# Performance work log

Hardware: AMD Instinct MI355X
Metric: run time of the kernel (lower is better)

## Reference

```python
import jax, jax.numpy as jnp
import numpy as np

B, C, H, W = 4, 128, 512, 512
K = 512          # num_kpt
NMS_R = 3        # nms_radius -> 7x7 window
NMS_ITER = 2


def _maxpool(x, r):
    # torch nn.MaxPool2d(kernel=2r+1, stride=1, padding=r) pads with -inf semantics
    return jax.lax.reduce_window(
        x, -jnp.inf, jax.lax.max,
        window_dimensions=(1, 1, 2 * r + 1, 2 * r + 1),
        window_strides=(1, 1, 1, 1),
        padding=((0, 0), (0, 0), (r, r), (r, r)))


def simple_nms(scores, r=NMS_R, iters=NMS_ITER):
    zeros = jnp.zeros_like(scores)
    max_mask = scores == _maxpool(scores, r)
    for _ in range(iters):
        supp_mask = _maxpool(max_mask.astype(scores.dtype), r) > 0
        supp_scores = jnp.where(supp_mask, zeros, scores)
        new_max_mask = supp_scores == _maxpool(supp_scores, r)
        max_mask = max_mask | (new_max_mask & ~supp_mask)
    return jnp.where(max_mask, scores, zeros)


def setup_inputs() -> dict:
    key = jax.random.key(0)
    k1, k2, k3 = jax.random.split(key, 3)
    score_bev = jax.random.uniform(k1, (B, 1, H, W), dtype=jnp.float32)
    feature_bev = jax.random.normal(k2, (B, C, H, W), dtype=jnp.float32)
    points = jax.random.normal(k3, (B, 4, H, W), dtype=jnp.float32)
    return {"score_bev": score_bev, "feature_bev": feature_bev, "points": points}


def reference(score_bev, feature_bev, points):
    # points[:,2]=0, points[:,3]=1 as in torch forward
    pts = points.at[:, 2].set(0.0).at[:, 3].set(1.0)

    nms = simple_nms(score_bev)                      # [B,1,H,W]
    s = score_bev[:, 0]                              # [B,H,W]
    sm = nms[:, 0]
    mask = (s == sm) & (s > 0)                       # NMS-surviving positive maxima

    # per-image top-k over valid candidates (invalid -> -1 sentinel, scores > 0)
    flat = jnp.where(mask, s, -1.0).reshape(B, H * W)
    _, idx = jax.lax.top_k(flat, K)                  # [B,K], sorted descending
    u, v = idx // W, idx % W                         # pixel coords

    kpts = jnp.take_along_axis(pts.reshape(B, 4, H * W), idx[:, None, :], axis=2)
    kpts = kpts.transpose(0, 2, 1)                   # [B,K,4]
    feas_kpt = jnp.take_along_axis(feature_bev.reshape(B, C, H * W), idx[:, None, :], axis=2)  # [B,C,K]
    pixels_kpt = jnp.stack([u, v], axis=-1)          # [B,K,2] int
    return kpts, feas_kpt, pixels_kpt
```

## Files before the change

### kernel.cpp

```cpp
#include <hip/hip_runtime.h>
#include <stdint.h>
#include <math.h>

#define BB 4
#define HH 512
#define WW 512
#define HWW (HH*WW)
#define CC 128
#define KK 512
#define SELCAP 2048
#define NBIN 8192
#define NPADK 512

#define TILE 64
#define HALO 15
#define TS 94
#define SWL 104
#define NT 1024
#define TCAP 512
#define NW2 16

typedef unsigned int uint;
typedef unsigned long long u64;

__device__ __forceinline__ float4 ldsf4(const float* p, int o){ return *(const float4*)(p + o); }

#define COLMAX7V(src, o, cm)                                                  \
    { float4 c0=ldsf4(src,(o)-3*SWL), c1=ldsf4(src,(o)-2*SWL), c2=ldsf4(src,(o)-SWL), \
             c3=ldsf4(src,(o)),       c4=ldsf4(src,(o)+SWL),   c5=ldsf4(src,(o)+2*SWL), \
             c6=ldsf4(src,(o)+3*SWL);                                         \
      cm.x=fmaxf(fmaxf(fmaxf(c0.x,c1.x),fmaxf(c2.x,c3.x)),fmaxf(fmaxf(c4.x,c5.x),c6.x)); \
      cm.y=fmaxf(fmaxf(fmaxf(c0.y,c1.y),fmaxf(c2.y,c3.y)),fmaxf(fmaxf(c4.y,c5.y),c6.y)); \
      cm.z=fmaxf(fmaxf(fmaxf(c0.z,c1.z),fmaxf(c2.z,c3.z)),fmaxf(fmaxf(c4.z,c5.z),c6.z)); \
      cm.w=fmaxf(fmaxf(fmaxf(c0.w,c1.w),fmaxf(c2.w,c3.w)),fmaxf(fmaxf(c4.w,c5.w),c6.w)); }

#define ROWMAXV(dst, src, Y0, NROW, G0, NG)                                   \
    for (int i = tid; i < (NROW)*(NG); i += NT){                              \
        int y = (Y0) + i/(NG);                                                \
        int o = y*SWL + (G0) + 4*(i%(NG)) + 4;                                \
        float4 va = ldsf4(src, o-4), vb = ldsf4(src, o), vc = ldsf4(src, o+4);\
        float m2a=fmaxf(va.y,va.z), m2b=fmaxf(va.w,vb.x), m2c=fmaxf(vb.y,vb.z),\
              m2d=fmaxf(vb.w,vc.x), m2e=fmaxf(vc.y,vc.z);                     \
        float4 r;                                                             \
        r.x = fmaxf(fmaxf(m2a,m2b), fmaxf(m2c, vb.w));                        \
        r.y = fmaxf(fmaxf(va.z,m2b), fmaxf(m2c, m2d));                        \
        r.z = fmaxf(fmaxf(m2b,m2c), fmaxf(m2d, vc.y));                        \
        r.w = fmaxf(fmaxf(vb.x,m2c), fmaxf(m2d, m2e));                        \
        *(float4*)((dst) + o) = r;                                            \
    }                                                                         \
    __syncthreads();

#define ROWORV(dst, src, Y0, NROW, G0, NG)                                    \
    for (int i = tid; i < (NROW)*(NG); i += NT){                              \
        int y = (Y0) + i/(NG);                                                \
        int o = y*SWL + (G0) + 4*(i%(NG)) + 4;                                \
        uint u0 = *(const uint*)((src)+o-4), u1 = *(const uint*)((src)+o),    \
             u2 = *(const uint*)((src)+o+4);                                  \
        u64 lo = (u64)u0 | ((u64)u1 << 32);                                   \
        uint r = (uint)(lo>>8) | (uint)(lo>>16) | (uint)(lo>>24) | (uint)(lo>>32) \
               | ((uint)(lo>>40)|(u2<<24)) | ((uint)(lo>>48)|(u2<<16))        \
               | ((uint)(lo>>56)|(u2<<8));                                    \
        *(uint*)((dst)+o) = r;                                                \
    }                                                                         \
    __syncthreads();

#define COLSUPPV(Y0, NROW, G0, NG)                                            \
    for (int i = tid; i < (NROW)*(NG); i += NT){                              \
        int y = (Y0) + i/(NG);                                                \
        int o = y*SWL + (G0) + 4*(i%(NG)) + 4;                                \
        uint v = *(const uint*)(T+o-3*SWL) | *(const uint*)(T+o-2*SWL)        \
               | *(const uint*)(T+o-SWL)   | *(const uint*)(T+o)              \
               | *(const uint*)(T+o+SWL)   | *(const uint*)(T+o+2*SWL)        \
               | *(const uint*)(T+o+3*SWL);                                   \
        *(uint*)(P + o) = v;                                                  \
        float4 s4 = ldsf4(S, o);                                              \
        float4 a;                                                             \
        a.x = (v & 0xffu)       ? 0.0f : s4.x;                                \
        a.y = (v & 0xff00u)     ? 0.0f : s4.y;                                \
        a.z = (v & 0xff0000u)   ? 0.0f : s4.z;                                \
        a.w = (v & 0xff000000u) ? 0.0f : s4.w;                                \
        *(float4*)(A + o) = a;                                                \
    }                                                                         \
    __syncthreads();

__global__ __launch_bounds__(NT) void nms_fused_k(const float* __restrict__ sc,
        float* __restrict__ cs, int* __restrict__ ci, int* __restrict__ cnt){
    __shared__ __align__(16) float S[TS*SWL];
    __shared__ __align__(16) float A[TS*SWL];
    __shared__ __align__(16) float Bf[TS*SWL];
    __shared__ __align__(16) unsigned char M[TS*SWL];
    __shared__ __align__(16) unsigned char T[TS*SWL];
    __shared__ __align__(16) unsigned char P[TS*SWL];
    __shared__ float lsc[TCAP];
    __shared__ int   lidx[TCAP];
    __shared__ int   lcnt;

    const int tid = threadIdx.x;
    const int bb = blockIdx.x >> 6;
    const int t  = blockIdx.x & 63;
    const int ty = t >> 3, tx = t & 7;
    const int oy = ty * TILE - HALO, ox = tx * TILE - HALO;
    const float* sb = sc + (size_t)bb * HWW;
    const float QNAN = __int_as_float(0x7fc00000);

    if (tid == 0) lcnt = 0;

    for (int i = tid; i < TS*SWL; i += NT){
        int y = i / SWL, x = i - y*SWL;
        int gy = oy + y, gx = ox + x - 4;
        float v = QNAN;
        if ((unsigned)gy < (unsigned)HH && (unsigned)gx < (unsigned)WW)
            v = sb[(gy << 9) + gx];
        S[i] = v;
    }
    __syncthreads();

    ROWMAXV(A, S, 0, 94, 0, 23)
    for (int i = tid; i < 88*23; i += NT){
        int y = 3 + i/23;
        int o = y*SWL + 4*(i%23) + 4;
        float4 cm; COLMAX7V(A, o, cm);
        float4 s4 = ldsf4(S, o);
        uint m = (s4.x==cm.x ?1u:0u) | (s4.y==cm.y ?0x100u:0u)
               | (s4.z==cm.z ?0x10000u:0u) | (s4.w==cm.w ?0x1000000u:0u);
        *(uint*)(M + o) = m;
    }
    __syncthreads();

    ROWORV(T, M, 3, 88, 4, 21)
    COLSUPPV(6, 82, 4, 21)
    ROWMAXV(Bf, A, 6, 82, 8, 20)
    for (int i = tid; i < 76*20; i += NT){
        int y = 9 + i/20;
        int o = y*SWL + 8 + 4*(i%20) + 4;
        float4 cm; COLMAX7V(Bf, o, cm);
        float4 a4 = ldsf4(A, o);
        uint p4 = *(const uint*)(P+o);
        uint nm = (a4.x==cm.x ?1u:0u)|(a4.y==cm.y ?0x100u:0u)
                | (a4.z==cm.z ?0x10000u:0u)|(a4.w==cm.w ?0x1000000u:0u);
        uint m4 = *(const uint*)(M+o);
        *(uint*)(M+o) = m4 | (nm & ~p4);
    }
    __syncthreads();

    ROWORV(T, M, 9, 76, 12, 18)
    COLSUPPV(12, 70, 12, 18)
    ROWMAXV(Bf, A, 12, 70, 12, 17)

    for (int i = tid; i < 64*17; i += NT){
        int y = 15 + i/17;
        int xg = 12 + 4*(i%17);
        int o = y*SWL + xg + 4;
        float4 cm; COLMAX7V(Bf, o, cm);
        float4 a4 = ldsf4(A, o), s4 = ldsf4(S, o);
        uint p4 = *(const uint*)(P+o), m4 = *(const uint*)(M+o);
        float sa[4] = {s4.x, s4.y, s4.z, s4.w};
        float aa[4] = {a4.x, a4.y, a4.z, a4.w};
        float ca[4] = {cm.x, cm.y, cm.z, cm.w};
        #pragma unroll
        for (int j = 0; j < 4; ++j){
            int x = xg + j;
            bool fm = ((m4 >> (8*j)) & 1u) || ((aa[j]==ca[j]) && !((p4 >> (8*j)) & 1u));
            if ((unsigned)(x - 15) < 64u && fm && sa[j] > 0.0f){
                int p = atomicAdd(&lcnt, 1);
                if (p < TCAP){ lsc[p] = sa[j]; lidx[p] = ((oy+y) << 9) + (ox+x); }
            }
        }
    }
    __syncthreads();

    int nl = lcnt; if (nl > TCAP) nl = TCAP;
    const int seg = bb * 64 + t;
    if (tid == 0) cnt[seg] = nl;
    float* os = cs + (size_t)seg * TCAP;
    int*   oi = ci + (size_t)seg * TCAP;
    for (int i = tid; i < nl; i += NT){ os[i] = lsc[i]; oi[i] = lidx[i]; }
}


__device__ __forceinline__ uint fxbin(float v){
    return ((uint)(v * 8388608.0f)) >> 10;
}

__global__ __launch_bounds__(NT) void selgather_k(
        const float* __restrict__ cs, const int* __restrict__ ci, const int* __restrict__ cnt,
        const float* __restrict__ pts, const float* __restrict__ feat,
        float* __restrict__ out){
    __shared__ int  hist[NBIN];
    __shared__ __align__(16) u64 keys[SELCAP + 4];
    __shared__ int  segc[64];
    __shared__ int  wsum[16];
    __shared__ int  sidx[KK];
    __shared__ uint sh_Tbits;
    __shared__ int  sh_bin, sh_kneed, sh_n, selCnt, bcnt;

    const int blk = blockIdx.x;
    const int b = blk >> 6, slice = blk & 63;
    const int tid = threadIdx.x;
    const int wv = tid >> 6, lane = tid & 63;

    {
        int4* h4 = (int4*)hist;
        for (int i = tid; i < NBIN/4; i += NT) h4[i] = make_int4(0,0,0,0);
    }
    if (tid < 64){ int c = cnt[b*64 + tid]; segc[tid] = (c > TCAP) ? TCAP : c; }
    if (tid == 0){ selCnt = 0; bcnt = 0; sh_Tbits = 1u; }
    __syncthreads();

    #pragma unroll
    for (int ss = 0; ss < 4; ++ss){
        int s = wv*4 + ss;
        int c = segc[s];
        const float* ps = cs + (size_t)(b*64 + s) * TCAP;
        for (int i = lane; i < c; i += 64)
            atomicAdd(&hist[fxbin(ps[i])], 1);
    }
    __syncthreads();

    int hh[8];
    {
        int4 h0 = *(int4*)&hist[tid*8], h1 = *(int4*)&hist[tid*8 + 4];
        hh[0]=h0.x; hh[1]=h0.y; hh[2]=h0.z; hh[3]=h0.w;
        hh[4]=h1.x; hh[5]=h1.y; hh[6]=h1.z; hh[7]=h1.w;
    }
    int s8 = hh[0]+hh[1]+hh[2]+hh[3]+hh[4]+hh[5]+hh[6]+hh[7];
    int suf = s8;
    #pragma unroll
    for (int off = 1; off < 64; off <<= 1){
        int v = __shfl_down(suf, off);
        if (lane + off < 64) suf += v;
    }
    if (lane == 0) wsum[wv] = suf;
    __syncthreads();
    int W = 0, tot = 0;
    #pragma unroll
    for (int w2 = 0; w2 < 16; ++w2){ int v = wsum[w2]; tot += v; if (w2 > wv) W += v; }
    if (tid == 0) sh_n = tot;
    int G = W + (suf - s8);
    if (tot >= KK && G < KK && G + s8 >= KK){
        int cum = G;
        #pragma unroll
        for (int k = 7; k >= 0; --k){
            if (cum + hh[k] >= KK){ sh_bin = tid*8 + k; sh_kneed = KK - cum; break; }
            cum += hh[k];
        }
    }
    __syncthreads();
    const int n = sh_n;

    uint Tbits = 1u;
    if (n >= KK){
        const int bstar = sh_bin, kneed = sh_kneed;
        #pragma unroll
        for (int ss = 0; ss < 4; ++ss){
            int s = wv*4 + ss;
            int c = segc[s];
            const float* ps = cs + (size_t)(b*64 + s) * TCAP;
            for (int i = lane; i < c; i += 64){
                float v = ps[i];
                if ((int)fxbin(v) == bstar){
                    int p = atomicAdd(&bcnt, 1);
                    if (p < SELCAP) keys[p] = (u64)__float_as_uint(v);
                }
            }
        }
        __syncthreads();
        int m = bcnt; if (m > SELCAP) m = SELCAP;
        if (tid < m){
            u64 mine = keys[tid];
            int gt = 0, ge = 0;
            for (int j = 0; j < m; ++j){
                u64 v = keys[j];
                gt += (v > mine) ? 1 : 0;
                ge += (v >= mine) ? 1 : 0;
            }
            if (gt < kneed && kneed <= ge) sh_Tbits = (uint)mine;
        }
        __syncthreads();
        Tbits = sh_Tbits;
    }

    #pragma unroll
    for (int ss = 0; ss < 4; ++ss){
        int s = wv*4 + ss;
        int c = segc[s];
        const float* ps = cs + (size_t)(b*64 + s) * TCAP;
        const int*   pi = ci + (size_t)(b*64 + s) * TCAP;
        for (int i0 = 0; i0 < c; i0 += 64){
            int i = i0 + lane;
            bool hit = false; uint bits = 0;
            if (i < c){ bits = __float_as_uint(ps[i]); hit = (bits >= Tbits); }
            u64 m = __ballot(hit);
            if (!m) continue;
            int wbase = 0;
            if (lane == 0) wbase = atomicAdd(&selCnt, (int)__popcll(m));
            wbase = __shfl(wbase, 0);
            if (hit){
                int p = wbase + (int)__popcll(m & ((1ull << lane) - 1ull));
                if (p < SELCAP) keys[p] = ((u64)bits << 32) | (uint)(~pi[i]);
            }
        }
    }
    __syncthreads();
    int ns = selCnt; if (ns > SELCAP) ns = SELCAP;
    for (int i = ns + tid; i < NPADK; i += NT) keys[i] = 0ull;
    __syncthreads();

    if (ns <= NPADK){
        u64 ck[8];
        #pragma unroll
        for (int r = 0; r < 8; ++r) ck[r] = keys[r*64 + lane];
        for (int t0 = 0; t0 < 32; ++t0){
            int t = wv*32 + t0;
            u64 my = keys[t];
            int c = 0;
            #pragma unroll
            for (int r = 0; r < 8; ++r) c += (ck[r] > my) ? 1 : 0;
            #pragma unroll
            for (int off = 1; off < 64; off <<= 1) c += __shfl_xor(c, off);
            if (lane == 0 && my != 0ull && c < KK)
                sidx[c] = (int)(~(uint)(my & 0xFFFFFFFFull));
        }
    } else {
        for (int i = tid; i < ns; i += NT){
            u64 my = keys[i];
            int rank = 0;
            for (int j = 0; j < ns; ++j) rank += (keys[j] > my) ? 1 : 0;
            if (rank < KK) sidx[rank] = (int)(~(uint)(my & 0xFFFFFFFFull));
        }
    }
    __syncthreads();

    if (ns < KK && tid == 0){
        int fill = ns;
        for (int idx = 0; idx < HWW && fill < KK; ++idx){
            bool inCand = false;
            for (int s = 0; s < 64 && !inCand; ++s){
                const int* pi = ci + (size_t)(b*64 + s) * TCAP;
                int c = segc[s];
                for (int i = 0; i < c; ++i) if (pi[i] == idx){ inCand = true; break; }
            }
            if (!inCand) sidx[fill++] = idx;
        }
    }
    __syncthreads();

    if (slice == 0){
        const float* pb = pts + (size_t)b * 4 * HWW;
        float* out0 = out + (size_t)b * KK * 4;
        float* out2 = out + (size_t)(BB * KK * 4 + BB * CC * KK) + (size_t)b * KK * 2;
        for (int k = tid; k < KK; k += NT){
            int idx = sidx[k];
            out0[k * 4 + 0] = pb[idx];
            out0[k * 4 + 1] = pb[HWW + idx];
            out0[k * 4 + 2] = 0.0f;
            out0[k * 4 + 3] = 1.0f;
            out2[k * 2 + 0] = (float)(idx >> 9);
            out2[k * 2 + 1] = (float)(idx & (WW - 1));
        }
    }
    {
        int j = slice * NT + tid;
        int c = j >> 9;
        int k = j & (KK - 1);
        float* out1 = out + (size_t)(BB * KK * 4) + (size_t)b * CC * KK;
        out1[j] = feat[(size_t)b * CC * HWW + (size_t)c * HWW + sidx[k]];
    }
}

extern "C" void kernel_launch(void* const* d_in, const int* in_sizes, int n_in,
                              void* d_out, int out_size, void* d_ws, size_t ws_size,
                              hipStream_t stream) {
    const float* s    = (const float*)d_in[0];
    const float* feat = (const float*)d_in[1];
    const float* pts  = (const float*)d_in[2];
    float* out = (float*)d_out;

    char* w = (char*)d_ws;
    float* cs  = (float*)w;  w += (size_t)BB * 64 * TCAP * 4;
    int*   ci  = (int*)w;    w += (size_t)BB * 64 * TCAP * 4;
    int*   cnt = (int*)w;    w += (size_t)BB * 64 * 4;

    nms_fused_k<<<BB * 64, NT, 0, stream>>>(s, cs, ci, cnt);
    selgather_k<<<BB * 64, NT, 0, stream>>>(cs, ci, cnt, pts, feat, out);
}
```

Measured before the change: 54.82 us.

## Use register sliding windows for row and column max/or passes in NMS

```diff
diff --git a/kernel.cpp b/kernel.cpp
--- a/kernel.cpp
+++ b/kernel.cpp
@@ -24,64 +24,62 @@
 typedef unsigned long long u64;
 
 __device__ __forceinline__ float4 ldsf4(const float* p, int o){ return *(const float4*)(p + o); }
-
-#define COLMAX7V(src, o, cm)                                                  \
-    { float4 c0=ldsf4(src,(o)-3*SWL), c1=ldsf4(src,(o)-2*SWL), c2=ldsf4(src,(o)-SWL), \
-             c3=ldsf4(src,(o)),       c4=ldsf4(src,(o)+SWL),   c5=ldsf4(src,(o)+2*SWL), \
-             c6=ldsf4(src,(o)+3*SWL);                                         \
-      cm.x=fmaxf(fmaxf(fmaxf(c0.x,c1.x),fmaxf(c2.x,c3.x)),fmaxf(fmaxf(c4.x,c5.x),c6.x)); \
-      cm.y=fmaxf(fmaxf(fmaxf(c0.y,c1.y),fmaxf(c2.y,c3.y)),fmaxf(fmaxf(c4.y,c5.y),c6.y)); \
-      cm.z=fmaxf(fmaxf(fmaxf(c0.z,c1.z),fmaxf(c2.z,c3.z)),fmaxf(fmaxf(c4.z,c5.z),c6.z)); \
-      cm.w=fmaxf(fmaxf(fmaxf(c0.w,c1.w),fmaxf(c2.w,c3.w)),fmaxf(fmaxf(c4.w,c5.w),c6.w)); }
-
-#define ROWMAXV(dst, src, Y0, NROW, G0, NG)                                   \
-    for (int i = tid; i < (NROW)*(NG); i += NT){                              \
-        int y = (Y0) + i/(NG);                                                \
-        int o = y*SWL + (G0) + 4*(i%(NG)) + 4;                                \
-        float4 va = ldsf4(src, o-4), vb = ldsf4(src, o), vc = ldsf4(src, o+4);\
-        float m2a=fmaxf(va.y,va.z), m2b=fmaxf(va.w,vb.x), m2c=fmaxf(vb.y,vb.z),\
-              m2d=fmaxf(vb.w,vc.x), m2e=fmaxf(vc.y,vc.z);                     \
-        float4 r;                                                             \
-        r.x = fmaxf(fmaxf(m2a,m2b), fmaxf(m2c, vb.w));                        \
-        r.y = fmaxf(fmaxf(va.z,m2b), fmaxf(m2c, m2d));                        \
-        r.z = fmaxf(fmaxf(m2b,m2c), fmaxf(m2d, vc.y));                        \
-        r.w = fmaxf(fmaxf(vb.x,m2c), fmaxf(m2d, m2e));                        \
-        *(float4*)((dst) + o) = r;                                            \
+__device__ __forceinline__ float4 f4max(float4 a, float4 b){
+    return make_float4(fmaxf(a.x,b.x), fmaxf(a.y,b.y), fmaxf(a.z,b.z), fmaxf(a.w,b.w));
+}
+
+#define ROWMAX_RUN(dst, src, Y0, NROW, G0, NG)                                \
+    { const int RUNS = ((NG) + 7) / 8;                                        \
+      for (int th = tid; th < (NROW)*RUNS; th += NT){                         \
+        int row = th / RUNS, u = th % RUNS;                                   \
+        int y = (Y0) + row, g0 = u*8;                                         \
+        int o0 = y*SWL + (G0) + 4*g0 + 4;                                     \
+        float4 Ax = ldsf4(src, o0-4), Bx = ldsf4(src, o0);                    \
+        _Pragma("unroll")                                                     \
+        for (int q = 0; q < 8; ++q){                                          \
+            if (g0 + q < (NG)){                                               \
+                int o = o0 + 4*q;                                             \
+                float4 Cx = ldsf4(src, o+4);                                  \
+                float m2a=fmaxf(Ax.y,Ax.z), m2b=fmaxf(Ax.w,Bx.x),             \
+                      m2c=fmaxf(Bx.y,Bx.z), m2d=fmaxf(Bx.w,Cx.x),             \
+                      m2e=fmaxf(Cx.y,Cx.z);                                   \
+                float4 r;                                                     \
+                r.x = fmaxf(fmaxf(m2a,m2b), fmaxf(m2c, Bx.w));                \
+                r.y = fmaxf(fmaxf(Ax.z,m2b), fmaxf(m2c, m2d));                \
+                r.z = fmaxf(fmaxf(m2b,m2c), fmaxf(m2d, Cx.y));                \
+                r.w = fmaxf(fmaxf(Bx.x,m2c), fmaxf(m2d, m2e));                \
+                *(float4*)((dst) + o) = r;                                    \
+                Ax = Bx; Bx = Cx;                                             \
+            }                                                                 \
+        }                                                                     \
+      }                                                                       \
     }                                                                         \
     __syncthreads();
 
-#define ROWORV(dst, src, Y0, NROW, G0, NG)                                    \
-    for (int i = tid; i < (NROW)*(NG); i += NT){                              \
-        int y = (Y0) + i/(NG);                                                \
-        int o = y*SWL + (G0) + 4*(i%(NG)) + 4;                                \
-        uint u0 = *(const uint*)((src)+o-4), u1 = *(const uint*)((src)+o),    \
-             u2 = *(const uint*)((src)+o+4);                                  \
-        u64 lo = (u64)u0 | ((u64)u1 << 32);                                   \
-        uint r = (uint)(lo>>8) | (uint)(lo>>16) | (uint)(lo>>24) | (uint)(lo>>32) \
-               | ((uint)(lo>>40)|(u2<<24)) | ((uint)(lo>>48)|(u2<<16))        \
-               | ((uint)(lo>>56)|(u2<<8));                                    \
-        *(uint*)((dst)+o) = r;                                                \
+#define ROWOR_RUN(dst, src, Y0, NROW, G0, NG)                                 \
+    { const int RUNS = ((NG) + 7) / 8;                                        \
+      for (int th = tid; th < (NROW)*RUNS; th += NT){                         \
+        int row = th / RUNS, u = th % RUNS;                                   \
+        int y = (Y0) + row, g0 = u*8;                                         \
+        int o0 = y*SWL + (G0) + 4*g0 + 4;                                     \
+        uint Au = *(const uint*)((src)+o0-4), Bu = *(const uint*)((src)+o0);  \
+        _Pragma("unroll")                                                     \
+        for (int q = 0; q < 8; ++q){                                          \
+            if (g0 + q < (NG)){                                               \
+                int o = o0 + 4*q;                                             \
+                uint Cu = *(const uint*)((src)+o+4);                          \
+                u64 lo = (u64)Au | ((u64)Bu << 32);                           \
+                uint r = (uint)(lo>>8) | (uint)(lo>>16) | (uint)(lo>>24)      \
+                       | (uint)(lo>>32) | ((uint)(lo>>40)|(Cu<<24))           \
+                       | ((uint)(lo>>48)|(Cu<<16)) | ((uint)(lo>>56)|(Cu<<8));\
+                *(uint*)((dst)+o) = r;                                        \
+                Au = Bu; Bu = Cu;                                             \
+            }                                                                 \
+        }                                                                     \
+      }                                                                       \
     }                                                                         \
     __syncthreads();
 
-#define COLSUPPV(Y0, NROW, G0, NG)                                            \
-    for (int i = tid; i < (NROW)*(NG); i += NT){                              \
-        int y = (Y0) + i/(NG);                                                \
-        int o = y*SWL + (G0) + 4*(i%(NG)) + 4;                                \
-        uint v = *(const uint*)(T+o-3*SWL) | *(const uint*)(T+o-2*SWL)        \
-               | *(const uint*)(T+o-SWL)   | *(const uint*)(T+o)              \
-               | *(const uint*)(T+o+SWL)   | *(const uint*)(T+o+2*SWL)        \
-               | *(const uint*)(T+o+3*SWL);                                   \
-        *(uint*)(P + o) = v;                                                  \
-        float4 s4 = ldsf4(S, o);                                              \
-        float4 a;                                                             \
-        a.x = (v & 0xffu)       ? 0.0f : s4.x;                                \
-        a.y = (v & 0xff00u)     ? 0.0f : s4.y;                                \
-        a.z = (v & 0xff0000u)   ? 0.0f : s4.z;                                \
-        a.w = (v & 0xff000000u) ? 0.0f : s4.w;                                \
-        *(float4*)(A + o) = a;                                                \
-    }                                                                         \
-    __syncthreads();
 
 __global__ __launch_bounds__(NT) void nms_fused_k(const float* __restrict__ sc,
         float* __restrict__ cs, int* __restrict__ ci, int* __restrict__ cnt){
@@ -115,56 +113,141 @@
     }
     __syncthreads();
 
-    ROWMAXV(A, S, 0, 94, 0, 23)
-    for (int i = tid; i < 88*23; i += NT){
-        int y = 3 + i/23;
-        int o = y*SWL + 4*(i%23) + 4;
-        float4 cm; COLMAX7V(A, o, cm);
-        float4 s4 = ldsf4(S, o);
-        uint m = (s4.x==cm.x ?1u:0u) | (s4.y==cm.y ?0x100u:0u)
-               | (s4.z==cm.z ?0x10000u:0u) | (s4.w==cm.w ?0x1000000u:0u);
-        *(uint*)(M + o) = m;
-    }
-    __syncthreads();
-
-    ROWORV(T, M, 3, 88, 4, 21)
-    COLSUPPV(6, 82, 4, 21)
-    ROWMAXV(Bf, A, 6, 82, 8, 20)
-    for (int i = tid; i < 76*20; i += NT){
-        int y = 9 + i/20;
-        int o = y*SWL + 8 + 4*(i%20) + 4;
-        float4 cm; COLMAX7V(Bf, o, cm);
-        float4 a4 = ldsf4(A, o);
-        uint p4 = *(const uint*)(P+o);
-        uint nm = (a4.x==cm.x ?1u:0u)|(a4.y==cm.y ?0x100u:0u)
-                | (a4.z==cm.z ?0x10000u:0u)|(a4.w==cm.w ?0x1000000u:0u);
-        uint m4 = *(const uint*)(M+o);
-        *(uint*)(M+o) = m4 | (nm & ~p4);
-    }
-    __syncthreads();
-
-    ROWORV(T, M, 9, 76, 12, 18)
-    COLSUPPV(12, 70, 12, 18)
-    ROWMAXV(Bf, A, 12, 70, 12, 17)
-
-    for (int i = tid; i < 64*17; i += NT){
-        int y = 15 + i/17;
-        int xg = 12 + 4*(i%17);
-        int o = y*SWL + xg + 4;
-        float4 cm; COLMAX7V(Bf, o, cm);
-        float4 a4 = ldsf4(A, o), s4 = ldsf4(S, o);
-        uint p4 = *(const uint*)(P+o), m4 = *(const uint*)(M+o);
-        float sa[4] = {s4.x, s4.y, s4.z, s4.w};
-        float aa[4] = {a4.x, a4.y, a4.z, a4.w};
-        float ca[4] = {cm.x, cm.y, cm.z, cm.w};
-        #pragma unroll
-        for (int j = 0; j < 4; ++j){
-            int x = xg + j;
-            bool fm = ((m4 >> (8*j)) & 1u) || ((aa[j]==ca[j]) && !((p4 >> (8*j)) & 1u));
-            if ((unsigned)(x - 15) < 64u && fm && sa[j] > 0.0f){
-                int p = atomicAdd(&lcnt, 1);
-                if (p < TCAP){ lsc[p] = sa[j]; lidx[p] = ((oy+y) << 9) + (ox+x); }
-            }
+    ROWMAX_RUN(A, S, 0, 94, 0, 23)
+
+    for (int th = tid; th < 11*23; th += NT){
+        int st = th / 23, g = th % 23;
+        int ys = 3 + st*8;
+        int xo = 4*g + 4;
+        float4 w0 = ldsf4(A,(ys-3)*SWL+xo), w1 = ldsf4(A,(ys-2)*SWL+xo),
+               w2 = ldsf4(A,(ys-1)*SWL+xo), w3 = ldsf4(A,(ys  )*SWL+xo),
+               w4 = ldsf4(A,(ys+1)*SWL+xo), w5 = ldsf4(A,(ys+2)*SWL+xo);
+        #pragma unroll
+        for (int r2 = 0; r2 < 8; ++r2){
+            int y = ys + r2;
+            float4 w6 = ldsf4(A,(y+3)*SWL+xo);
+            float4 cm = f4max(f4max(f4max(w0,w1),f4max(w2,w3)), f4max(f4max(w4,w5),w6));
+            float4 s4 = ldsf4(S, y*SWL+xo);
+            uint m = (s4.x==cm.x?1u:0u)|(s4.y==cm.y?0x100u:0u)
+                   | (s4.z==cm.z?0x10000u:0u)|(s4.w==cm.w?0x1000000u:0u);
+            *(uint*)(M + y*SWL+xo) = m;
+            w0=w1; w1=w2; w2=w3; w3=w4; w4=w5; w5=w6;
+        }
+    }
+    __syncthreads();
+
+    ROWOR_RUN(T, M, 3, 88, 4, 21)
+
+    for (int th = tid; th < 14*21; th += NT){
+        int st = th / 21, g = th % 21;
+        int ys = 6 + st*6;
+        int xo = 4*g + 8;
+        uint t0 = *(uint*)(T+(ys-3)*SWL+xo), t1 = *(uint*)(T+(ys-2)*SWL+xo),
+             t2 = *(uint*)(T+(ys-1)*SWL+xo), t3 = *(uint*)(T+(ys  )*SWL+xo),
+             t4 = *(uint*)(T+(ys+1)*SWL+xo), t5 = *(uint*)(T+(ys+2)*SWL+xo);
+        #pragma unroll
+        for (int r2 = 0; r2 < 6; ++r2){
+            int y = ys + r2;
+            if (y < 88){
+                uint t6 = *(uint*)(T+(y+3)*SWL+xo);
+                uint v = t0|t1|t2|t3|t4|t5|t6;
+                *(uint*)(P + y*SWL+xo) = v;
+                float4 s4 = ldsf4(S, y*SWL+xo);
+                float4 a;
+                a.x = (v & 0xffu)       ? 0.0f : s4.x;
+                a.y = (v & 0xff00u)     ? 0.0f : s4.y;
+                a.z = (v & 0xff0000u)   ? 0.0f : s4.z;
+                a.w = (v & 0xff000000u) ? 0.0f : s4.w;
+                *(float4*)(A + y*SWL+xo) = a;
+                t0=t1; t1=t2; t2=t3; t3=t4; t4=t5; t5=t6;
+            }
+        }
+    }
+    __syncthreads();
+
+    ROWMAX_RUN(Bf, A, 6, 82, 8, 20)
+
+    for (int th = tid; th < 19*20; th += NT){
+        int st = th / 20, g = th % 20;
+        int ys = 9 + st*4;
+        int xo = 4*g + 12;
+        float4 w0 = ldsf4(Bf,(ys-3)*SWL+xo), w1 = ldsf4(Bf,(ys-2)*SWL+xo),
+               w2 = ldsf4(Bf,(ys-1)*SWL+xo), w3 = ldsf4(Bf,(ys  )*SWL+xo),
+               w4 = ldsf4(Bf,(ys+1)*SWL+xo), w5 = ldsf4(Bf,(ys+2)*SWL+xo);
+        #pragma unroll
+        for (int r2 = 0; r2 < 4; ++r2){
+            int y = ys + r2;
+            float4 w6 = ldsf4(Bf,(y+3)*SWL+xo);
+            float4 cm = f4max(f4max(f4max(w0,w1),f4max(w2,w3)), f4max(f4max(w4,w5),w6));
+            float4 a4 = ldsf4(A, y*SWL+xo);
+            uint p4 = *(uint*)(P + y*SWL+xo);
+            uint nm = (a4.x==cm.x?1u:0u)|(a4.y==cm.y?0x100u:0u)
+                    | (a4.z==cm.z?0x10000u:0u)|(a4.w==cm.w?0x1000000u:0u);
+            uint m4 = *(uint*)(M + y*SWL+xo);
+            *(uint*)(M + y*SWL+xo) = m4 | (nm & ~p4);
+            w0=w1; w1=w2; w2=w3; w3=w4; w4=w5; w5=w6;
+        }
+    }
+    __syncthreads();
+
+    ROWOR_RUN(T, M, 9, 76, 12, 18)
+
+    for (int th = tid; th < 10*18; th += NT){
+        int st = th / 18, g = th % 18;
+        int ys = 12 + st*7;
+        int xo = 4*g + 16;
+        uint t0 = *(uint*)(T+(ys-3)*SWL+xo), t1 = *(uint*)(T+(ys-2)*SWL+xo),
+             t2 = *(uint*)(T+(ys-1)*SWL+xo), t3 = *(uint*)(T+(ys  )*SWL+xo),
+             t4 = *(uint*)(T+(ys+1)*SWL+xo), t5 = *(uint*)(T+(ys+2)*SWL+xo);
+        #pragma unroll
+        for (int r2 = 0; r2 < 7; ++r2){
+            int y = ys + r2;
+            if (y < 82){
+                uint t6 = *(uint*)(T+(y+3)*SWL+xo);
+                uint v = t0|t1|t2|t3|t4|t5|t6;
+                *(uint*)(P + y*SWL+xo) = v;
+                float4 s4 = ldsf4(S, y*SWL+xo);
+                float4 a;
+                a.x = (v & 0xffu)       ? 0.0f : s4.x;
+                a.y = (v & 0xff00u)     ? 0.0f : s4.y;
+                a.z = (v & 0xff0000u)   ? 0.0f : s4.z;
+                a.w = (v & 0xff000000u) ? 0.0f : s4.w;
+                *(float4*)(A + y*SWL+xo) = a;
+                t0=t1; t1=t2; t2=t3; t3=t4; t4=t5; t5=t6;
+            }
+        }
+    }
+    __syncthreads();
+
+    ROWMAX_RUN(Bf, A, 12, 70, 12, 17)
+
+    for (int th = tid; th < 8*17; th += NT){
+        int st = th / 17, g = th % 17;
+        int ys = 15 + st*8;
+        int xo = 4*g + 16;
+        float4 w0 = ldsf4(Bf,(ys-3)*SWL+xo), w1 = ldsf4(Bf,(ys-2)*SWL+xo),
+               w2 = ldsf4(Bf,(ys-1)*SWL+xo), w3 = ldsf4(Bf,(ys  )*SWL+xo),
+               w4 = ldsf4(Bf,(ys+1)*SWL+xo), w5 = ldsf4(Bf,(ys+2)*SWL+xo);
+        #pragma unroll
+        for (int r2 = 0; r2 < 8; ++r2){
+            int y = ys + r2;
+            float4 w6 = ldsf4(Bf,(y+3)*SWL+xo);
+            float4 cm = f4max(f4max(f4max(w0,w1),f4max(w2,w3)), f4max(f4max(w4,w5),w6));
+            float4 a4 = ldsf4(A, y*SWL+xo), s4 = ldsf4(S, y*SWL+xo);
+            uint p4 = *(uint*)(P + y*SWL+xo), m4 = *(uint*)(M + y*SWL+xo);
+            float sa[4] = {s4.x, s4.y, s4.z, s4.w};
+            float aa[4] = {a4.x, a4.y, a4.z, a4.w};
+            float ca[4] = {cm.x, cm.y, cm.z, cm.w};
+            #pragma unroll
+            for (int j = 0; j < 4; ++j){
+                int x = xo - 4 + j;
+                bool fm = ((m4 >> (8*j)) & 1u) || ((aa[j]==ca[j]) && !((p4 >> (8*j)) & 1u));
+                if ((unsigned)(x - 15) < 64u && fm && sa[j] > 0.0f){
+                    int p = atomicAdd(&lcnt, 1);
+                    if (p < TCAP){ lsc[p] = sa[j]; lidx[p] = ((oy+y) << 9) + (ox+x); }
+                }
+            }
+            w0=w1; w1=w2; w2=w3; w3=w4; w4=w5; w5=w6;
         }
     }
     __syncthreads();
```

Result: slower. 57.71 us (+5.3%).
